# Optimization experiments

Measured on AMD Instinct MI355X. Metric: run time of the kernel, lower is better.

Reference implementation:

```python
import jax, jax.numpy as jnp
import numpy as np

B, T, D_MODEL, WINDOW = 2, 2048, 512, 32


def setup_inputs() -> dict:
    key = jax.random.key(0)
    ks = jax.random.split(key, 5)
    s = 1.0 / np.sqrt(D_MODEL)
    x = jax.random.normal(ks[0], (B, T, D_MODEL), jnp.float32)
    # torch.nn.Linear convention: weight [out_features, in_features], y = x @ W.T + b
    w_qkv = jax.random.uniform(ks[1], (3 * D_MODEL, D_MODEL), jnp.float32, -s, s)
    b_qkv = jax.random.uniform(ks[2], (3 * D_MODEL,), jnp.float32, -s, s)
    w_proj = jax.random.uniform(ks[3], (D_MODEL, D_MODEL), jnp.float32, -s, s)
    b_proj = jax.random.uniform(ks[4], (D_MODEL,), jnp.float32, -s, s)
    return {"x": x, "w_qkv": w_qkv, "b_qkv": b_qkv, "w_proj": w_proj, "b_proj": b_proj}


def reference(x, w_qkv, b_qkv, w_proj, b_proj):
    Bb, Tt, C = x.shape
    qkv = x @ w_qkv.T + b_qkv                      # [B,T,3C]
    q, k, v = jnp.split(qkv, 3, axis=-1)           # each [B,T,C]
    W = 2 * WINDOW - 1                             # non-causal window span [t-w+1, t+w-1]
    offs = jnp.arange(W) - (WINDOW - 1)            # [W]
    idx = jnp.arange(Tt)[:, None] + offs[None, :]  # [T,W] absolute key positions
    valid = (idx >= 0) & (idx < Tt)                # mask out-of-range window slots
    idx_c = jnp.clip(idx, 0, Tt - 1)
    k_win = k[:, idx_c]                            # [B,T,W,C]
    v_win = v[:, idx_c]                            # [B,T,W,C]
    scale = jnp.asarray(C, x.dtype) ** 0.5
    scores = jnp.einsum('btc,btwc->btw', q, k_win) / scale
    scores = jnp.where(valid[None], scores, -jnp.inf)
    p = jax.nn.softmax(scores, axis=-1)            # [B,T,W]
    out = jnp.einsum('btw,btwc->btc', p, v_win)    # [B,T,C]
    return out @ w_proj.T + b_proj
```

## Files before the change

### kernel.cpp

```cpp
#include <hip/hip_runtime.h>
#include <math.h>

#define BB 2
#define TT 2048
#define CC 512
#define WIN 32
#define WSZ 63
#define MM (BB * TT)
#define QKLD 1024

typedef __attribute__((ext_vector_type(8))) short short8;
typedef __attribute__((ext_vector_type(4))) float floatx4;

__device__ inline unsigned short bf16_rn(float f) {
  unsigned u = __builtin_bit_cast(unsigned, f);
  u += 0x7fff + ((u >> 16) & 1);
  return (unsigned short)(u >> 16);
}
__device__ inline unsigned pack_bf16x2(float lo, float hi) {
  return (unsigned)bf16_rn(lo) | ((unsigned)bf16_rn(hi) << 16);
}

#define NX  (MM * CC)
#define NWQ (3 * CC * CC)
#define NWP (CC * CC)
#define NXBLK (NX / 2048)

__global__ __launch_bounds__(256) void convert_bf16(
    const float* __restrict__ x, const float* __restrict__ wq,
    const float* __restrict__ wp, ushort* __restrict__ xb,
    ushort* __restrict__ wqb, ushort* __restrict__ wpb) {
  int blk = blockIdx.x;
  if (blk < NXBLK) blk = ((blk & 7) << 7) | (blk >> 3);
  const size_t e = ((size_t)blk * 256 + threadIdx.x) * 8;
  const float* src;
  ushort* dst;
  size_t off;
  if (e < NX) { src = x; dst = xb; off = e; }
  else if (e < NX + NWQ) { src = wq; dst = wqb; off = e - NX; }
  else { src = wp; dst = wpb; off = e - NX - NWQ; }
  float4 v0 = ((const float4*)(src + off))[0];
  float4 v1 = ((const float4*)(src + off))[1];
  uint4 o;
  o.x = pack_bf16x2(v0.x, v0.y);
  o.y = pack_bf16x2(v0.z, v0.w);
  o.z = pack_bf16x2(v1.x, v1.y);
  o.w = pack_bf16x2(v1.z, v1.w);
  *(uint4*)(dst + off) = o;
}

#define PSTR 264
#define VSTR 136

__global__ __launch_bounds__(256, 3) void gemm_qkv(
    const ushort* __restrict__ A, const ushort* __restrict__ B,
    const float* __restrict__ bias, ushort* __restrict__ C,
    ushort* __restrict__ VT) {
  __shared__ __align__(16) ushort Bs[64 * PSTR];

  const int tid = threadIdx.x;
  const int lane = tid & 63;
  const int wave = tid >> 6;
  const int blk = blockIdx.x;
  const int xcd = blk & 7, j = blk >> 3;
  const int m0 = (xcd * 4 + (j & 3)) * 128;
  const int n0 = (j >> 2) * 64;
  const int wm = wave * 32;
  const int mlane = lane & 15, quad = lane >> 4;

  floatx4 acc[2][4];
#pragma unroll
  for (int i = 0; i < 2; ++i)
#pragma unroll
    for (int jj = 0; jj < 4; ++jj) acc[i][jj] = (floatx4){0.f, 0.f, 0.f, 0.f};

  for (int h = 0; h < 2; ++h) {
    if (h) __syncthreads();
#pragma unroll
    for (int i = 0; i < 8; ++i) {
      const int idx = tid + 256 * i;
      const int r = idx >> 5, kc = (idx & 31) * 8;
      *(uint4*)(&Bs[r * PSTR + kc]) =
          *(const uint4*)(B + (size_t)(n0 + r) * CC + h * 256 + kc);
    }
    short8 apre[16];
#pragma unroll
    for (int ks = 0; ks < 8; ++ks)
#pragma unroll
      for (int mi = 0; mi < 2; ++mi)
        apre[ks * 2 + mi] = *(const short8*)(
            A + (size_t)(m0 + wm + mi * 16 + mlane) * CC + h * 256 + ks * 32 + quad * 8);
    __syncthreads();
#pragma unroll
    for (int ks = 0; ks < 8; ++ks) {
      short8 bfr[4];
#pragma unroll
      for (int ni = 0; ni < 4; ++ni)
        bfr[ni] = *(const short8*)(&Bs[(ni * 16 + mlane) * PSTR + ks * 32 + quad * 8]);
#pragma unroll
      for (int mi = 0; mi < 2; ++mi)
#pragma unroll
        for (int ni = 0; ni < 4; ++ni)
          acc[mi][ni] = __builtin_amdgcn_mfma_f32_16x16x32_bf16(
              apre[ks * 2 + mi], bfr[ni], acc[mi][ni], 0, 0, 0);
    }
  }

  if (n0 < 1024) {
#pragma unroll
    for (int ni = 0; ni < 4; ++ni) {
      const int n = n0 + ni * 16 + mlane;
      const float bn = bias[n];
#pragma unroll
      for (int mi = 0; mi < 2; ++mi) {
        const int mbase = m0 + wm + mi * 16 + quad * 4;
#pragma unroll
        for (int r = 0; r < 4; ++r)
          C[(size_t)(mbase + r) * QKLD + n] = bf16_rn(acc[mi][ni][r] + bn);
      }
    }
  } else {
    ushort* Vt = Bs;
    __syncthreads();
#pragma unroll
    for (int ni = 0; ni < 4; ++ni) {
      const int n_l = ni * 16 + mlane;
      const float bn = bias[n0 + n_l];
#pragma unroll
      for (int mi = 0; mi < 2; ++mi) {
        const int m_l = wm + mi * 16 + quad * 4;
        ushort4 pk;
        pk.x = bf16_rn(acc[mi][ni][0] + bn);
        pk.y = bf16_rn(acc[mi][ni][1] + bn);
        pk.z = bf16_rn(acc[mi][ni][2] + bn);
        pk.w = bf16_rn(acc[mi][ni][3] + bn);
        *(ushort4*)(&Vt[n_l * VSTR + m_l]) = pk;
      }
    }
    __syncthreads();
#pragma unroll
    for (int i = 0; i < 4; ++i) {
      const int idx = tid + 256 * i;
      const int n_l = idx >> 4, mo = (idx & 15) * 8;
      *(uint4*)(VT + (size_t)(n0 - 1024 + n_l) * MM + m0 + mo) =
          *(const uint4*)(&Vt[n_l * VSTR + mo]);
    }
  }
}

#define ATILE 16
#define SLD 100
#define PLD 104
#define ATS 520

__global__ __launch_bounds__(512, 2) void attn_proj(
    const ushort* __restrict__ qkv, const ushort* __restrict__ vT,
    const ushort* __restrict__ wpb, const float* __restrict__ bproj,
    float* __restrict__ out) {
  __shared__ __align__(16) float s_s[16 * SLD];
  __shared__ __align__(16) ushort p_s[16 * PLD];
  __shared__ __align__(16) ushort at_s[16 * ATS];

  const int tid = threadIdx.x;
  const int wave = tid >> 6, lane = tid & 63;
  const int mlane = lane & 15, quad = lane >> 4;
  const int blk = blockIdx.x;
  const int grp = ((blk & 7) << 5) | (blk >> 3);
  const int bt0 = grp * ATILE;
  const int b = bt0 / TT, t0 = bt0 % TT;
  const ushort* qbase = qkv + (size_t)b * TT * QKLD;

  if (wave < 6) {
    const ushort* qrow = qbase + (ptrdiff_t)(t0 + mlane) * QKLD;
    const ushort* krow = qbase + (ptrdiff_t)(t0 - 32 + wave * 16 + mlane) * QKLD + CC;
    short8 qa[16], ka[16];
#pragma unroll
    for (int ks = 0; ks < 16; ++ks) {
      qa[ks] = *(const short8*)(qrow + ks * 32 + quad * 8);
      ka[ks] = *(const short8*)(krow + ks * 32 + quad * 8);
    }
    floatx4 sa = (floatx4){0.f, 0.f, 0.f, 0.f}, sb = sa;
#pragma unroll
    for (int ks = 0; ks < 16; ks += 2) {
      sa = __builtin_amdgcn_mfma_f32_16x16x32_bf16(qa[ks], ka[ks], sa, 0, 0, 0);
      sb = __builtin_amdgcn_mfma_f32_16x16x32_bf16(qa[ks + 1], ka[ks + 1], sb, 0, 0, 0);
    }
#pragma unroll
    for (int r = 0; r < 4; ++r)
      s_s[(quad * 4 + r) * SLD + wave * 16 + mlane] = sa[r] + sb[r];
  }
  __syncthreads();

  {
    const int row = tid >> 5, l5 = tid & 31;
    const float inv_scale = 0.044194173824159216f;
    float e[3];
    float mx = -INFINITY;
#pragma unroll
    for (int i = 0; i < 3; ++i) {
      const int r = l5 + 32 * i;
      const int j = r - 1 - row;
      const int src = t0 - 32 + r;
      const bool valid = (j >= 0) && (j < WSZ) && (src >= 0) && (src < TT);
      e[i] = valid ? s_s[row * SLD + r] * inv_scale : -INFINITY;
      mx = fmaxf(mx, e[i]);
    }
    mx = fmaxf(mx, __shfl_xor(mx, 1));  mx = fmaxf(mx, __shfl_xor(mx, 2));
    mx = fmaxf(mx, __shfl_xor(mx, 4));  mx = fmaxf(mx, __shfl_xor(mx, 8));
    mx = fmaxf(mx, __shfl_xor(mx, 16));
    float sum = 0.f;
#pragma unroll
    for (int i = 0; i < 3; ++i) {
      e[i] = (e[i] == -INFINITY) ? 0.f : __expf(e[i] - mx);
      sum += e[i];
    }
    sum += __shfl_xor(sum, 1); sum += __shfl_xor(sum, 2);
    sum += __shfl_xor(sum, 4); sum += __shfl_xor(sum, 8);
    sum += __shfl_xor(sum, 16);
    const float rs = 1.f / sum;
#pragma unroll
    for (int i = 0; i < 3; ++i)
      p_s[row * PLD + l5 + 32 * i] = bf16_rn(e[i] * rs);
    if (l5 < 8) p_s[row * PLD + 96 + l5] = 0;
  }
  __syncthreads();

  const ptrdiff_t mcol0 = (ptrdiff_t)b * TT + t0 - 32;
  {
    short8 pa[3];
#pragma unroll
    for (int ks = 0; ks < 3; ++ks)
      pa[ks] = *(const short8*)(&p_s[mlane * PLD + ks * 32 + quad * 8]);
    short8 vv[4][3];
#pragma unroll
    for (int i = 0; i < 4; ++i) {
      const ushort* vrow = vT + (ptrdiff_t)((wave * 4 + i) * 16 + mlane) * MM + mcol0;
#pragma unroll
      for (int ks = 0; ks < 3; ++ks)
        vv[i][ks] = *(const short8*)(vrow + ks * 32 + quad * 8);
    }
#pragma unroll
    for (int i = 0; i < 4; ++i) {
      const int nt = wave * 4 + i;
      floatx4 o = (floatx4){0.f, 0.f, 0.f, 0.f};
#pragma unroll
      for (int ks = 0; ks < 3; ++ks)
        o = __builtin_amdgcn_mfma_f32_16x16x32_bf16(pa[ks], vv[i][ks], o, 0, 0, 0);
#pragma unroll
      for (int r = 0; r < 4; ++r)
        at_s[(quad * 4 + r) * ATS + nt * 16 + mlane] = bf16_rn(o[r]);
    }
  }
  __syncthreads();

  {
    short8 af[16];
#pragma unroll
    for (int ks = 0; ks < 16; ++ks)
      af[ks] = *(const short8*)(&at_s[mlane * ATS + ks * 32 + quad * 8]);
#pragma unroll
    for (int i = 0; i < 4; ++i) {
      const int n = (wave * 4 + i) * 16 + mlane;
      const ushort* wrow = wpb + (size_t)n * CC;
      short8 bfr[16];
#pragma unroll
      for (int ks = 0; ks < 16; ++ks)
        bfr[ks] = *(const short8*)(wrow + ks * 32 + quad * 8);
      floatx4 oa = (floatx4){0.f, 0.f, 0.f, 0.f}, ob = oa;
#pragma unroll
      for (int ks = 0; ks < 16; ks += 2) {
        oa = __builtin_amdgcn_mfma_f32_16x16x32_bf16(af[ks], bfr[ks], oa, 0, 0, 0);
        ob = __builtin_amdgcn_mfma_f32_16x16x32_bf16(af[ks + 1], bfr[ks + 1], ob, 0, 0, 0);
      }
      const float bn = bproj[n];
#pragma unroll
      for (int r = 0; r < 4; ++r)
        out[(size_t)(bt0 + quad * 4 + r) * CC + n] = oa[r] + ob[r] + bn;
    }
  }
}

extern "C" void kernel_launch(void* const* d_in, const int* in_sizes, int n_in,
                              void* d_out, int out_size, void* d_ws, size_t ws_size,
                              hipStream_t stream) {
  const float* x      = (const float*)d_in[0];
  const float* w_qkv  = (const float*)d_in[1];
  const float* b_qkv  = (const float*)d_in[2];
  const float* w_proj = (const float*)d_in[3];
  const float* b_proj = (const float*)d_in[4];
  float* outp = (float*)d_out;

  ushort* base  = (ushort*)d_ws;
  ushort* qkv   = base + 131072;
  ushort* xb    = qkv + (size_t)MM * QKLD;
  ushort* wqb   = xb + (size_t)NX;
  ushort* wpb   = wqb + (size_t)NWQ;
  ushort* vTg   = wpb + (size_t)NWP;
  ushort* vT    = vTg + 64;

  convert_bf16<<<(NX + NWQ + NWP) / (256 * 8), 256, 0, stream>>>(x, w_qkv, w_proj, xb, wqb, wpb);
  gemm_qkv<<<768, 256, 0, stream>>>(xb, wqb, b_qkv, qkv, vT);
  attn_proj<<<256, 512, 0, stream>>>(qkv, vT, wpb, b_proj, outp);
}
```

Before: 115.3 us.

## Fuse QKV projection into attention kernel with inter-block flag synchronization

Removes the separate x-to-bf16 conversion and the QKV GEMM kernel. Each attention block now converts its own 16 rows of x in registers and computes their Q, K and V. Q stays in LDS, while K and transposed V go to global memory for neighbouring blocks. Blocks publish a release flag and spin-wait on the flags of adjacent tiles before the windowed attention. The aim is to cut the launch count and the full qkv intermediate round trip, at the cost of every block streaming the whole QKV weight matrix straight from global/L2 with a skinny M=16 MFMA shape. The flags are never reset between calls, so a repeated launch could read stale K/V from the previous call.

```diff
diff --git a/kernel.cpp b/kernel.cpp
--- a/kernel.cpp
+++ b/kernel.cpp
@@ -7,7 +7,9 @@
 #define WIN 32
 #define WSZ 63
 #define MM (BB * TT)
-#define QKLD 1024
+#define NWQ (3 * CC * CC)
+#define NWP (CC * CC)
+#define MAGIC 0x13572468
 
 typedef __attribute__((ext_vector_type(8))) short short8;
 typedef __attribute__((ext_vector_type(4))) float floatx4;
@@ -21,24 +23,15 @@
   return (unsigned)bf16_rn(lo) | ((unsigned)bf16_rn(hi) << 16);
 }
 
-#define NX  (MM * CC)
-#define NWQ (3 * CC * CC)
-#define NWP (CC * CC)
-#define NXBLK (NX / 2048)
-
-__global__ __launch_bounds__(256) void convert_bf16(
-    const float* __restrict__ x, const float* __restrict__ wq,
-    const float* __restrict__ wp, ushort* __restrict__ xb,
+__global__ __launch_bounds__(256) void convert_w(
+    const float* __restrict__ wq, const float* __restrict__ wp,
     ushort* __restrict__ wqb, ushort* __restrict__ wpb) {
-  int blk = blockIdx.x;
-  if (blk < NXBLK) blk = ((blk & 7) << 7) | (blk >> 3);
-  const size_t e = ((size_t)blk * 256 + threadIdx.x) * 8;
+  const size_t e = ((size_t)blockIdx.x * 256 + threadIdx.x) * 8;
   const float* src;
   ushort* dst;
   size_t off;
-  if (e < NX) { src = x; dst = xb; off = e; }
-  else if (e < NX + NWQ) { src = wq; dst = wqb; off = e - NX; }
-  else { src = wp; dst = wpb; off = e - NX - NWQ; }
+  if (e < NWQ) { src = wq; dst = wqb; off = e; }
+  else { src = wp; dst = wpb; off = e - NWQ; }
   float4 v0 = ((const float4*)(src + off))[0];
   float4 v1 = ((const float4*)(src + off))[1];
   uint4 o;
@@ -49,136 +42,122 @@
   *(uint4*)(dst + off) = o;
 }
 
-#define PSTR 264
-#define VSTR 136
-
-__global__ __launch_bounds__(256, 3) void gemm_qkv(
-    const ushort* __restrict__ A, const ushort* __restrict__ B,
-    const float* __restrict__ bias, ushort* __restrict__ C,
-    ushort* __restrict__ VT) {
-  __shared__ __align__(16) ushort Bs[64 * PSTR];
-
-  const int tid = threadIdx.x;
-  const int lane = tid & 63;
-  const int wave = tid >> 6;
-  const int blk = blockIdx.x;
-  const int xcd = blk & 7, j = blk >> 3;
-  const int m0 = (xcd * 4 + (j & 3)) * 128;
-  const int n0 = (j >> 2) * 64;
-  const int wm = wave * 32;
-  const int mlane = lane & 15, quad = lane >> 4;
-
-  floatx4 acc[2][4];
-#pragma unroll
-  for (int i = 0; i < 2; ++i)
-#pragma unroll
-    for (int jj = 0; jj < 4; ++jj) acc[i][jj] = (floatx4){0.f, 0.f, 0.f, 0.f};
-
-  for (int h = 0; h < 2; ++h) {
-    if (h) __syncthreads();
-#pragma unroll
-    for (int i = 0; i < 8; ++i) {
-      const int idx = tid + 256 * i;
-      const int r = idx >> 5, kc = (idx & 31) * 8;
-      *(uint4*)(&Bs[r * PSTR + kc]) =
-          *(const uint4*)(B + (size_t)(n0 + r) * CC + h * 256 + kc);
-    }
-    short8 apre[16];
-#pragma unroll
-    for (int ks = 0; ks < 8; ++ks)
-#pragma unroll
-      for (int mi = 0; mi < 2; ++mi)
-        apre[ks * 2 + mi] = *(const short8*)(
-            A + (size_t)(m0 + wm + mi * 16 + mlane) * CC + h * 256 + ks * 32 + quad * 8);
-    __syncthreads();
-#pragma unroll
-    for (int ks = 0; ks < 8; ++ks) {
-      short8 bfr[4];
-#pragma unroll
-      for (int ni = 0; ni < 4; ++ni)
-        bfr[ni] = *(const short8*)(&Bs[(ni * 16 + mlane) * PSTR + ks * 32 + quad * 8]);
-#pragma unroll
-      for (int mi = 0; mi < 2; ++mi)
-#pragma unroll
-        for (int ni = 0; ni < 4; ++ni)
-          acc[mi][ni] = __builtin_amdgcn_mfma_f32_16x16x32_bf16(
-              apre[ks * 2 + mi], bfr[ni], acc[mi][ni], 0, 0, 0);
-    }
-  }
-
-  if (n0 < 1024) {
-#pragma unroll
-    for (int ni = 0; ni < 4; ++ni) {
-      const int n = n0 + ni * 16 + mlane;
-      const float bn = bias[n];
-#pragma unroll
-      for (int mi = 0; mi < 2; ++mi) {
-        const int mbase = m0 + wm + mi * 16 + quad * 4;
-#pragma unroll
-        for (int r = 0; r < 4; ++r)
-          C[(size_t)(mbase + r) * QKLD + n] = bf16_rn(acc[mi][ni][r] + bn);
-      }
-    }
-  } else {
-    ushort* Vt = Bs;
-    __syncthreads();
-#pragma unroll
-    for (int ni = 0; ni < 4; ++ni) {
-      const int n_l = ni * 16 + mlane;
-      const float bn = bias[n0 + n_l];
-#pragma unroll
-      for (int mi = 0; mi < 2; ++mi) {
-        const int m_l = wm + mi * 16 + quad * 4;
-        ushort4 pk;
-        pk.x = bf16_rn(acc[mi][ni][0] + bn);
-        pk.y = bf16_rn(acc[mi][ni][1] + bn);
-        pk.z = bf16_rn(acc[mi][ni][2] + bn);
-        pk.w = bf16_rn(acc[mi][ni][3] + bn);
-        *(ushort4*)(&Vt[n_l * VSTR + m_l]) = pk;
-      }
-    }
-    __syncthreads();
-#pragma unroll
-    for (int i = 0; i < 4; ++i) {
-      const int idx = tid + 256 * i;
-      const int n_l = idx >> 4, mo = (idx & 15) * 8;
-      *(uint4*)(VT + (size_t)(n0 - 1024 + n_l) * MM + m0 + mo) =
-          *(const uint4*)(&Vt[n_l * VSTR + mo]);
-    }
-  }
-}
-
-#define ATILE 16
 #define SLD 100
 #define PLD 104
-#define ATS 520
-
-__global__ __launch_bounds__(512, 2) void attn_proj(
-    const ushort* __restrict__ qkv, const ushort* __restrict__ vT,
-    const ushort* __restrict__ wpb, const float* __restrict__ bproj,
+
+__global__ __launch_bounds__(512) void fused_attn(
+    const float* __restrict__ x, const ushort* __restrict__ wqb,
+    const float* __restrict__ bqkv, const ushort* __restrict__ wpb,
+    const float* __restrict__ bproj, ushort* __restrict__ kglob,
+    ushort* __restrict__ vT, int* __restrict__ flags,
     float* __restrict__ out) {
-  __shared__ __align__(16) float s_s[16 * SLD];
-  __shared__ __align__(16) ushort p_s[16 * PLD];
-  __shared__ __align__(16) ushort at_s[16 * ATS];
+  __shared__ __align__(16) ushort QS[16 * 520];
+  __shared__ __align__(16) char tbraw[20480];
+  ushort* kbuf = (ushort*)tbraw;
+  ushort* vbuf = (ushort*)tbraw;
+  float*  s_s  = (float*)tbraw;
+  ushort* p_s  = (ushort*)(tbraw + 16 * SLD * 4);
 
   const int tid = threadIdx.x;
   const int wave = tid >> 6, lane = tid & 63;
   const int mlane = lane & 15, quad = lane >> 4;
   const int blk = blockIdx.x;
   const int grp = ((blk & 7) << 5) | (blk >> 3);
-  const int bt0 = grp * ATILE;
+  const int bt0 = grp * 16;
   const int b = bt0 / TT, t0 = bt0 % TT;
-  const ushort* qbase = qkv + (size_t)b * TT * QKLD;
+
+  short8 af[16];
+  const float* xrow = x + (size_t)(bt0 + mlane) * CC;
+#pragma unroll
+  for (int ks = 0; ks < 16; ++ks) {
+    float4 u0 = *(const float4*)(xrow + ks * 32 + quad * 8);
+    float4 u1 = *(const float4*)(xrow + ks * 32 + quad * 8 + 4);
+    uint4 pk = make_uint4(pack_bf16x2(u0.x, u0.y), pack_bf16x2(u0.z, u0.w),
+                          pack_bf16x2(u1.x, u1.y), pack_bf16x2(u1.z, u1.w));
+    af[ks] = __builtin_bit_cast(short8, pk);
+  }
+  floatx4 acc[12];
+#pragma unroll
+  for (int j = 0; j < 12; ++j) acc[j] = (floatx4){0.f, 0.f, 0.f, 0.f};
+#pragma unroll
+  for (int j = 0; j < 12; ++j) {
+    const int nt = wave + 8 * j;
+    const ushort* wrow = wqb + (size_t)(nt * 16 + mlane) * CC;
+#pragma unroll
+    for (int ks = 0; ks < 16; ++ks) {
+      short8 bfr = *(const short8*)(wrow + ks * 32 + quad * 8);
+      acc[j] = __builtin_amdgcn_mfma_f32_16x16x32_bf16(af[ks], bfr, acc[j], 0, 0, 0);
+    }
+  }
+
+#pragma unroll
+  for (int j = 0; j < 4; ++j) {
+    const int nt = wave + 8 * j;
+    const float bn = bqkv[nt * 16 + mlane];
+#pragma unroll
+    for (int r = 0; r < 4; ++r)
+      QS[(quad * 4 + r) * 520 + nt * 16 + mlane] = bf16_rn(acc[j][r] + bn);
+  }
+#pragma unroll
+  for (int j = 4; j < 8; ++j) {
+    const int nt = wave + 8 * j;
+    const float bn = bqkv[nt * 16 + mlane];
+#pragma unroll
+    for (int r = 0; r < 4; ++r)
+      kbuf[(quad * 4 + r) * 520 + (nt - 32) * 16 + mlane] = bf16_rn(acc[j][r] + bn);
+  }
+  __syncthreads();
+#pragma unroll
+  for (int i = 0; i < 2; ++i) {
+    const int idx = tid + 512 * i;
+    const int row = idx >> 6, c8 = (idx & 63) * 8;
+    *(uint4*)(kglob + (size_t)(bt0 + row) * CC + c8) = *(const uint4*)(&kbuf[row * 520 + c8]);
+  }
+  __syncthreads();
+#pragma unroll
+  for (int j = 8; j < 12; ++j) {
+    const int nt = wave + 8 * j;
+    const int c = (nt - 64) * 16 + mlane;
+    const float bn = bqkv[1024 + c];
+    ushort4 pk4;
+    pk4.x = bf16_rn(acc[j][0] + bn);
+    pk4.y = bf16_rn(acc[j][1] + bn);
+    pk4.z = bf16_rn(acc[j][2] + bn);
+    pk4.w = bf16_rn(acc[j][3] + bn);
+    *(ushort4*)(&vbuf[c * 20 + quad * 4]) = pk4;
+  }
+  __syncthreads();
+  {
+    const int c = tid;
+    uint4 a0 = *(const uint4*)(&vbuf[c * 20]);
+    uint4 a1 = *(const uint4*)(&vbuf[c * 20 + 8]);
+    *(uint4*)(vT + (size_t)c * MM + bt0) = a0;
+    *(uint4*)(vT + (size_t)c * MM + bt0 + 8) = a1;
+  }
+  __threadfence();
+  __syncthreads();
+  if (tid == 0)
+    __hip_atomic_store(&flags[grp], MAGIC, __ATOMIC_RELEASE, __HIP_MEMORY_SCOPE_AGENT);
+  if (lane == 0) {
+    const int gb = b * (TT / 16);
+#pragma unroll
+    for (int d = -2; d <= 2; ++d) {
+      int gn = grp + d;
+      gn = (gn < gb) ? gb : ((gn > gb + 127) ? gb + 127 : gn);
+      while (__hip_atomic_load(&flags[gn], __ATOMIC_ACQUIRE, __HIP_MEMORY_SCOPE_AGENT) != MAGIC) {}
+    }
+  }
+  __syncthreads();
 
   if (wave < 6) {
-    const ushort* qrow = qbase + (ptrdiff_t)(t0 + mlane) * QKLD;
-    const ushort* krow = qbase + (ptrdiff_t)(t0 - 32 + wave * 16 + mlane) * QKLD + CC;
     short8 qa[16], ka[16];
 #pragma unroll
-    for (int ks = 0; ks < 16; ++ks) {
-      qa[ks] = *(const short8*)(qrow + ks * 32 + quad * 8);
+    for (int ks = 0; ks < 16; ++ks)
+      qa[ks] = *(const short8*)(&QS[mlane * 520 + ks * 32 + quad * 8]);
+    const ushort* krow = kglob + (ptrdiff_t)(b * TT + t0 - 32 + wave * 16 + mlane) * CC;
+#pragma unroll
+    for (int ks = 0; ks < 16; ++ks)
       ka[ks] = *(const short8*)(krow + ks * 32 + quad * 8);
-    }
     floatx4 sa = (floatx4){0.f, 0.f, 0.f, 0.f}, sb = sa;
 #pragma unroll
     for (int ks = 0; ks < 16; ks += 2) {
@@ -248,29 +227,27 @@
         o = __builtin_amdgcn_mfma_f32_16x16x32_bf16(pa[ks], vv[i][ks], o, 0, 0, 0);
 #pragma unroll
       for (int r = 0; r < 4; ++r)
-        at_s[(quad * 4 + r) * ATS + nt * 16 + mlane] = bf16_rn(o[r]);
-    }
-  }
-  __syncthreads();
-
-  {
-    short8 af[16];
+        QS[(quad * 4 + r) * 520 + nt * 16 + mlane] = bf16_rn(o[r]);
+    }
+  }
+  __syncthreads();
+
+  {
+    short8 pf[16];
 #pragma unroll
     for (int ks = 0; ks < 16; ++ks)
-      af[ks] = *(const short8*)(&at_s[mlane * ATS + ks * 32 + quad * 8]);
+      pf[ks] = *(const short8*)(&QS[mlane * 520 + ks * 32 + quad * 8]);
 #pragma unroll
     for (int i = 0; i < 4; ++i) {
       const int n = (wave * 4 + i) * 16 + mlane;
       const ushort* wrow = wpb + (size_t)n * CC;
-      short8 bfr[16];
-#pragma unroll
-      for (int ks = 0; ks < 16; ++ks)
-        bfr[ks] = *(const short8*)(wrow + ks * 32 + quad * 8);
       floatx4 oa = (floatx4){0.f, 0.f, 0.f, 0.f}, ob = oa;
 #pragma unroll
       for (int ks = 0; ks < 16; ks += 2) {
-        oa = __builtin_amdgcn_mfma_f32_16x16x32_bf16(af[ks], bfr[ks], oa, 0, 0, 0);
-        ob = __builtin_amdgcn_mfma_f32_16x16x32_bf16(af[ks + 1], bfr[ks + 1], ob, 0, 0, 0);
+        short8 b0 = *(const short8*)(wrow + ks * 32 + quad * 8);
+        short8 b1 = *(const short8*)(wrow + (ks + 1) * 32 + quad * 8);
+        oa = __builtin_amdgcn_mfma_f32_16x16x32_bf16(pf[ks], b0, oa, 0, 0, 0);
+        ob = __builtin_amdgcn_mfma_f32_16x16x32_bf16(pf[ks + 1], b1, ob, 0, 0, 0);
       }
       const float bn = bproj[n];
 #pragma unroll
@@ -291,14 +268,14 @@
   float* outp = (float*)d_out;
 
   ushort* base  = (ushort*)d_ws;
-  ushort* qkv   = base + 131072;
-  ushort* xb    = qkv + (size_t)MM * QKLD;
-  ushort* wqb   = xb + (size_t)NX;
+  int*    flags = (int*)d_ws;
+  ushort* kglob = base + 131072;
+  ushort* wqb   = kglob + (size_t)MM * CC;
   ushort* wpb   = wqb + (size_t)NWQ;
   ushort* vTg   = wpb + (size_t)NWP;
   ushort* vT    = vTg + 64;
 
-  convert_bf16<<<(NX + NWQ + NWP) / (256 * 8), 256, 0, stream>>>(x, w_qkv, w_proj, xb, wqb, wpb);
-  gemm_qkv<<<768, 256, 0, stream>>>(xb, wqb, b_qkv, qkv, vT);
-  attn_proj<<<256, 512, 0, stream>>>(qkv, vT, wpb, b_proj, outp);
-}
+  convert_w<<<(NWQ + NWP) / (256 * 8), 256, 0, stream>>>(w_qkv, w_proj, wqb, wpb);
+  fused_attn<<<256, 512, 0, stream>>>(x, wqb, b_qkv, wpb, b_proj,
+                                      kglob, vT, flags, outp);
+}
```

New measurement: 298.1 us. 159% more time.
